# Kernel tuning notes

Hardware: AMD Instinct MI355X
Metric: run time of the kernel (lower is better)

The kernel has to match this reference:

```python
import jax, jax.numpy as jnp
import numpy as np

TAU = 2.0        # spikingjelly LIFNode default tau
VTH = 1.0        # v_threshold
ALPHA = 2.0      # ATan surrogate alpha
NUM_HEADS = 8
N_WIN = 8
TOPK = 4


@jax.custom_vjp
def atan_heaviside(x):
    # spike = H(v - v_th), with ATan surrogate gradient
    return (x >= 0.0).astype(x.dtype)

def _ah_fwd(x):
    return atan_heaviside(x), x

def _ah_bwd(x, g):
    half_pi_alpha = np.float32(np.pi / 2.0 * ALPHA)
    return (g * (ALPHA / 2.0) / (1.0 + (half_pi_alpha * x) ** 2),)

atan_heaviside.defvjp(_ah_fwd, _ah_bwd)


def lif(x):
    """Multi-step LIF over leading time dim. decay_input=True, v_reset=0, detach_reset."""
    def step(v, xt):
        v = v + (xt - v) / TAU                      # charge
        s = atan_heaviside(v - VTH)                 # fire
        v = v * (1.0 - jax.lax.stop_gradient(s))    # hard reset (detached)
        return v, s
    _, spikes = jax.lax.scan(step, jnp.zeros_like(x[0]), x)
    return spikes


def setup_inputs() -> dict:
    key = jax.random.key(0)
    k1, k2, k3, k4, k5 = jax.random.split(key, 5)
    T, B, L, C = 4, 4, 1024, 256
    x = jax.random.normal(k1, (T, B, L, C), dtype=jnp.float32)
    w_qkv = jax.random.normal(k2, (C, 3 * C), dtype=jnp.float32) * (C ** -0.5)
    b_qkv = jax.random.normal(k3, (3 * C,), dtype=jnp.float32) * 0.02
    w_proj = jax.random.normal(k4, (C, C), dtype=jnp.float32) * (C ** -0.5)
    b_proj = jax.random.normal(k5, (C,), dtype=jnp.float32) * 0.02
    return {"x": x, "w_qkv": w_qkv, "b_qkv": b_qkv, "w_proj": w_proj, "b_proj": b_proj}


def reference(x, w_qkv, b_qkv, w_proj, b_proj):
    T, B, L, C = x.shape
    hd = C // NUM_HEADS
    win = L // N_WIN
    scale = hd ** -0.5

    # --- region-level routing (on raw input summed over time) ---
    xs = x.sum(axis=0).reshape(B, N_WIN, win, C)
    region = xs.sum(axis=2)                                  # [B, n_win, C]
    attn_r = jnp.einsum('bnc,bmc->bnm', region, region) * (C ** -0.5)
    _, idx = jax.lax.top_k(attn_r, TOPK)                     # [B, n_win, topk] int32

    # --- qkv + LIF spiking ---
    qkv = x @ w_qkv + b_qkv                                  # [T,B,L,3C]
    q, k, v = jnp.split(qkv, 3, axis=-1)
    q, k, v = lif(q), lif(k), lif(v)
    q = q.reshape(T, B, N_WIN, win, NUM_HEADS, hd)
    k = k.reshape(T, B, N_WIN, win, NUM_HEADS, hd)
    v = v.reshape(T, B, N_WIN, win, NUM_HEADS, hd)

    # --- gather routed KV windows (vectorized; topk-major concat like torch.cat) ---
    b_idx = jnp.arange(B)[:, None, None]                     # [B,1,1]
    k_g = k[:, b_idx, idx].reshape(T, B, N_WIN, TOPK * win, NUM_HEADS, hd)
    v_g = v[:, b_idx, idx].reshape(T, B, N_WIN, TOPK * win, NUM_HEADS, hd)

    # --- windowed attention over gathered keys ---
    attn = jnp.einsum('tbnqhd,tbnkhd->tbnhqk', q, k_g) * scale
    attn = jax.nn.softmax(attn, axis=-1)
    out = jnp.einsum('tbnhqk,tbnkhd->tbnqhd', attn, v_g).reshape(T, B, L, C)

    out = lif(out @ w_proj + b_proj)
    return out
```

## Files before the change

### kernel.cpp

```cpp
#include <hip/hip_runtime.h>
#include <cstdint>
#include <cstddef>

#define TT 4
#define BB 4
#define LL 1024
#define CC 256
#define HH 8
#define HD 32
#define NWIN 8
#define WIN 128
#define TOPKN 4
#define C3 768
#define PKW 24

__global__ __launch_bounds__(64) void region_kernel(const float* __restrict__ x,
                                                    float* __restrict__ region) {
    int bn = blockIdx.x;
    int b = bn >> 3, n = bn & 7;
    int c = blockIdx.y * 64 + threadIdx.x;
    float tot = 0.0f;
    for (int r = 0; r < WIN; ++r) {
        int l = n * WIN + r;
        float s = 0.0f;
        for (int t = 0; t < TT; ++t) {
            s += x[(((size_t)t * BB + b) * LL + l) * CC + c];
        }
        tot += s;
    }
    region[(size_t)bn * CC + c] = tot;
}

__global__ __launch_bounds__(64) void route_kernel(const float* __restrict__ region,
                                                   int* __restrict__ idx) {
    int b = blockIdx.x;
    __shared__ float reg[NWIN][CC];
    __shared__ float attn_r[NWIN][NWIN];
    int tid = threadIdx.x;
    for (int e = tid; e < NWIN * CC; e += 64)
        reg[e >> 8][e & 255] = region[(size_t)b * NWIN * CC + e];
    __syncthreads();
    int n = tid >> 3, m = tid & 7;
    float s = 0.0f;
    for (int c = 0; c < CC; ++c) s += reg[n][c] * reg[m][c];
    attn_r[n][m] = s * 0.0625f;
    __syncthreads();
    if (tid < NWIN) {
        float vals[NWIN];
        for (int m2 = 0; m2 < NWIN; ++m2) vals[m2] = attn_r[tid][m2];
        for (int kk = 0; kk < TOPKN; ++kk) {
            int bi = 0; float bv = vals[0];
            for (int m2 = 1; m2 < NWIN; ++m2) {
                if (vals[m2] > bv) { bv = vals[m2]; bi = m2; }
            }
            idx[(b * NWIN + tid) * TOPKN + kk] = bi;
            vals[bi] = -INFINITY;
        }
    }
}

__global__ __launch_bounds__(256, 3) void gemm_bias128(const float* __restrict__ A,
                                                       const float* __restrict__ W,
                                                       const float* __restrict__ bias,
                                                       float* __restrict__ C,
                                                       int M, int N, int K) {
    const int BM = 128, BN = 128, BK = 16, TM = 8;
    __shared__ float As[BK][BM + 4];
    __shared__ float Bs[BK][136];
    int tid = threadIdx.x;
    int tx = tid & 15, ty = tid >> 4;
    int bm = blockIdx.x * BM, bn = blockIdx.y * BN;
    float acc[TM][8] = {};
    for (int k0 = 0; k0 < K; k0 += BK) {
#pragma unroll
        for (int it = 0; it < 2; ++it) {
            int i = it * 256 + tid;
            int row = i >> 2, kc = (i & 3) * 4;
            float4 v = *(const float4*)(A + (size_t)(bm + row) * K + k0 + kc);
            As[kc + 0][row] = v.x; As[kc + 1][row] = v.y;
            As[kc + 2][row] = v.z; As[kc + 3][row] = v.w;
        }
#pragma unroll
        for (int it = 0; it < 2; ++it) {
            int i = it * 256 + tid;
            int kr = i >> 5, nc = (i & 31) * 4;
            float4 v = *(const float4*)(W + (size_t)(k0 + kr) * N + bn + nc);
            *(float4*)&Bs[kr][nc] = v;
        }
        __syncthreads();
#pragma unroll
        for (int kk = 0; kk < BK; ++kk) {
            float a[TM], bb[8];
            const float4* ap = (const float4*)&As[kk][ty * TM];
            float4 a0 = ap[0], a1 = ap[1];
            a[0]=a0.x; a[1]=a0.y; a[2]=a0.z; a[3]=a0.w;
            a[4]=a1.x; a[5]=a1.y; a[6]=a1.z; a[7]=a1.w;
            float4 b0 = *(const float4*)&Bs[kk][tx * 4];
            float4 b1 = *(const float4*)&Bs[kk][64 + tx * 4];
            bb[0]=b0.x; bb[1]=b0.y; bb[2]=b0.z; bb[3]=b0.w;
            bb[4]=b1.x; bb[5]=b1.y; bb[6]=b1.z; bb[7]=b1.w;
#pragma unroll
            for (int i = 0; i < TM; ++i)
#pragma unroll
                for (int j = 0; j < 8; ++j)
                    acc[i][j] = fmaf(a[i], bb[j], acc[i][j]);
        }
        __syncthreads();
    }
#pragma unroll
    for (int i = 0; i < TM; ++i) {
        int row = bm + ty * TM + i;
        int col0 = bn + tx * 4;
        int col1 = bn + 64 + tx * 4;
        float4 o0 = make_float4(acc[i][0] + bias[col0 + 0], acc[i][1] + bias[col0 + 1],
                                acc[i][2] + bias[col0 + 2], acc[i][3] + bias[col0 + 3]);
        float4 o1 = make_float4(acc[i][4] + bias[col1 + 0], acc[i][5] + bias[col1 + 1],
                                acc[i][6] + bias[col1 + 2], acc[i][7] + bias[col1 + 3]);
        *(float4*)&C[(size_t)row * N + col0] = o0;
        *(float4*)&C[(size_t)row * N + col1] = o1;
    }
}

__global__ __launch_bounds__(256, 4) void gemm_bias64(const float* __restrict__ A,
                                                      const float* __restrict__ W,
                                                      const float* __restrict__ bias,
                                                      float* __restrict__ C,
                                                      int M, int N, int K) {
    const int BM = 64, BN = 64, BK = 16;
    __shared__ float As[BK][BM + 4];
    __shared__ float Bs[BK][72];
    int tid = threadIdx.x;
    int tx = tid & 15, ty = tid >> 4;
    int bm = blockIdx.x * BM, bn = blockIdx.y * BN;
    float acc[4][4] = {};
    for (int k0 = 0; k0 < K; k0 += BK) {
        {
            int row = tid >> 2, kc = (tid & 3) * 4;
            float4 v = *(const float4*)(A + (size_t)(bm + row) * K + k0 + kc);
            As[kc + 0][row] = v.x; As[kc + 1][row] = v.y;
            As[kc + 2][row] = v.z; As[kc + 3][row] = v.w;
        }
        {
            int kr = tid >> 4, nc = (tid & 15) * 4;
            float4 v = *(const float4*)(W + (size_t)(k0 + kr) * N + bn + nc);
            *(float4*)&Bs[kr][nc] = v;
        }
        __syncthreads();
#pragma unroll
        for (int kk = 0; kk < BK; ++kk) {
            float4 av = *(const float4*)&As[kk][ty * 4];
            float4 bv = *(const float4*)&Bs[kk][tx * 4];
            float a[4] = {av.x, av.y, av.z, av.w};
            float bb[4] = {bv.x, bv.y, bv.z, bv.w};
#pragma unroll
            for (int i = 0; i < 4; ++i)
#pragma unroll
                for (int j = 0; j < 4; ++j)
                    acc[i][j] = fmaf(a[i], bb[j], acc[i][j]);
        }
        __syncthreads();
    }
#pragma unroll
    for (int i = 0; i < 4; ++i) {
        int row = bm + ty * 4 + i;
        int col = bn + tx * 4;
        float4 o = make_float4(acc[i][0] + bias[col + 0], acc[i][1] + bias[col + 1],
                               acc[i][2] + bias[col + 2], acc[i][3] + bias[col + 3]);
        *(float4*)&C[(size_t)row * N + col] = o;
    }
}

__global__ __launch_bounds__(256) void lif_kernel(const float* src, float* dst, size_t stride) {
    size_t i = ((size_t)blockIdx.x * blockDim.x + threadIdx.x) * 4;
    float v[4] = {0.f, 0.f, 0.f, 0.f};
    for (int t = 0; t < TT; ++t) {
        float4 xv4 = *(const float4*)(src + (size_t)t * stride + i);
        float xv[4] = {xv4.x, xv4.y, xv4.z, xv4.w};
        float sp[4];
#pragma unroll
        for (int j = 0; j < 4; ++j) {
            v[j] = v[j] + (xv[j] - v[j]) * 0.5f;
            bool fire = (v[j] >= 1.0f);
            sp[j] = fire ? 1.0f : 0.0f;
            v[j] = fire ? 0.0f : v[j];
        }
        *(float4*)(dst + (size_t)t * stride + i) = make_float4(sp[0], sp[1], sp[2], sp[3]);
    }
}

__global__ __launch_bounds__(192) void lif_pack_kernel(const float* __restrict__ qkv,
                                                       uint32_t* __restrict__ pk) {
    int row = blockIdx.x;
    int tid = threadIdx.x;
    int c = tid * 4;
    int wid = tid >> 6;
    int lane = tid & 63;
    const size_t stride = (size_t)BB * LL * C3;
    const float* base = qkv + (size_t)row * C3 + c;

    float v[4] = {0.f, 0.f, 0.f, 0.f};
    for (int t = 0; t < TT; ++t) {
        float4 xv4 = *(const float4*)(base + (size_t)t * stride);
        float xv[4] = {xv4.x, xv4.y, xv4.z, xv4.w};
        bool fire[4];
#pragma unroll
        for (int j = 0; j < 4; ++j) {
            v[j] = v[j] + (xv[j] - v[j]) * 0.5f;
            fire[j] = (v[j] >= 1.0f);
            v[j] = fire[j] ? 0.0f : v[j];
        }
        unsigned long long B0 = __ballot(fire[0]);
        unsigned long long B1 = __ballot(fire[1]);
        unsigned long long B2 = __ballot(fire[2]);
        unsigned long long B3 = __ballot(fire[3]);
        if (lane < 8) {
            uint32_t word = ((uint32_t)(B0 >> (8 * lane)) & 0xFFu)
                          | (((uint32_t)(B1 >> (8 * lane)) & 0xFFu) << 8)
                          | (((uint32_t)(B2 >> (8 * lane)) & 0xFFu) << 16)
                          | (((uint32_t)(B3 >> (8 * lane)) & 0xFFu) << 24);
            pk[((size_t)t * BB * LL + row) * PKW + wid * 8 + lane] = word;
        }
    }
}

__global__ __launch_bounds__(256, 2) void attn_pv(const uint32_t* __restrict__ pk,
                                                  const int* __restrict__ idxws,
                                                  float* __restrict__ out) {
    int bid = blockIdx.x;
    int hp = bid & 3, n = (bid >> 2) & 7, b = (bid >> 5) & 3, t = bid >> 7;
    __shared__ float ptab[33][256];
    __shared__ uint32_t kbs[2][512];
    __shared__ uint32_t vbs[2][512];
    int tid = threadIdx.x;
    int qg = tid & 31, dh = (tid >> 5) & 3, h = tid >> 7;
    int lbase = (t * BB + b) * LL;

    const int* ip = idxws + (b * NWIN + n) * TOPKN;
    int s0r = ip[0], s1r = ip[1], s2r = ip[2], s3r = ip[3];

#pragma unroll 4
    for (int e = tid; e < 1024; e += 256) {
        int hh = e >> 9, kk = e & 511;
        int w = kk >> 7;
        int sw = (w == 0) ? s0r : (w == 1) ? s1r : (w == 2) ? s2r : s3r;
        size_t rowb = (size_t)(lbase + sw * WIN + (kk & 127)) * PKW + hp * 2 + hh;
        kbs[hh][kk] = pk[rowb + 8];
        vbs[hh][kk] = pk[rowb + 16];
    }
    uint32_t qw[4];
#pragma unroll
    for (int j = 0; j < 4; ++j)
        qw[j] = pk[(size_t)(lbase + n * WIN + qg + 32 * j) * PKW + hp * 2 + h];
    __syncthreads();

    const float ALPHA_SC = 0.17677669529663687f;
    {
        int qq = tid & 127, hu = tid >> 7;
        uint32_t qwt = pk[(size_t)(lbase + n * WIN + qq) * PKW + hp * 2 + hu];
        const uint4* kb4u = (const uint4*)kbs[hu];
        int smax = 0;
#pragma unroll 8
        for (int k4 = 0; k4 < 128; ++k4) {
            uint4 w4 = kb4u[k4];
            smax = max(smax, __popc(qwt & w4.x));
            smax = max(smax, __popc(qwt & w4.y));
            smax = max(smax, __popc(qwt & w4.z));
            smax = max(smax, __popc(qwt & w4.w));
        }
        float am = __fmul_rn((float)smax, ALPHA_SC);
        for (int s = 0; s <= 32; ++s)
            ptab[s][tid] = expf(__fsub_rn(__fmul_rn((float)s, ALPHA_SC), am));
        float Z = 0.0f;
#pragma unroll 4
        for (int k4 = 0; k4 < 128; ++k4) {
            uint4 w4 = kb4u[k4];
            Z += ptab[__popc(qwt & w4.x)][tid];
            Z += ptab[__popc(qwt & w4.y)][tid];
            Z += ptab[__popc(qwt & w4.z)][tid];
            Z += ptab[__popc(qwt & w4.w)][tid];
        }
        for (int s = 0; s <= 32; ++s)
            ptab[s][tid] = ptab[s][tid] / Z;
    }
    __syncthreads();

    const uint4* kb4 = (const uint4*)kbs[h];
    const uint32_t* vbh = vbs[h];
    int c0 = h * 128 + qg;
    int po = 2 * dh;
    float acc[4][8];
#pragma unroll
    for (int j = 0; j < 4; ++j)
#pragma unroll
        for (int e = 0; e < 8; ++e) acc[j][e] = 0.0f;

#pragma unroll 1
    for (int g = 0; g < 128; ++g) {
        uint4 kw = kb4[g];
#pragma unroll
        for (int r = 0; r < 4; ++r) {
            uint32_t krow = (r == 0) ? kw.x : (r == 1) ? kw.y : (r == 2) ? kw.z : kw.w;
            uint32_t sh = vbh[g * 4 + r] >> po;
            float P0 = ptab[__popc(qw[0] & krow)][c0];
            float P1 = ptab[__popc(qw[1] & krow)][c0 + 32];
            float P2 = ptab[__popc(qw[2] & krow)][c0 + 64];
            float P3 = ptab[__popc(qw[3] & krow)][c0 + 96];
#pragma unroll
            for (int e = 0; e < 8; ++e) {
                const int offs = (e & 3) * 8 + (e >> 2);
                float vf = (float)((sh >> offs) & 1u);
                acc[0][e] = fmaf(P0, vf, acc[0][e]);
                acc[1][e] = fmaf(P1, vf, acc[1][e]);
                acc[2][e] = fmaf(P2, vf, acc[2][e]);
                acc[3][e] = fmaf(P3, vf, acc[3][e]);
            }
        }
    }

#pragma unroll
    for (int j = 0; j < 4; ++j) {
        size_t ob = (size_t)(lbase + n * WIN + qg + 32 * j) * CC
                    + (hp * 2 + h) * 32 + dh * 8;
        *(float4*)&out[ob]     = make_float4(acc[j][0], acc[j][1], acc[j][2], acc[j][3]);
        *(float4*)&out[ob + 4] = make_float4(acc[j][4], acc[j][5], acc[j][6], acc[j][7]);
    }
}

extern "C" void kernel_launch(void* const* d_in, const int* in_sizes, int n_in,
                              void* d_out, int out_size, void* d_ws, size_t ws_size,
                              hipStream_t stream) {
    const float* x      = (const float*)d_in[0];
    const float* w_qkv  = (const float*)d_in[1];
    const float* b_qkv  = (const float*)d_in[2];
    const float* w_proj = (const float*)d_in[3];
    const float* b_proj = (const float*)d_in[4];
    float* ws = (float*)d_ws;

    float* qkv      = ws;
    float* attn_out = ws + 12582912;
    float* proj     = ws + 16777216;
    uint32_t* pkb   = (uint32_t*)proj;
    float* region   = ws + 20971520;
    int*   idxp     = (int*)(ws + 20979712);
    float* outp     = (float*)d_out;

    region_kernel<<<dim3(BB * NWIN, 4), dim3(64), 0, stream>>>(x, region);
    route_kernel<<<dim3(BB), dim3(64), 0, stream>>>(region, idxp);
    gemm_bias128<<<dim3(128, 6), dim3(256), 0, stream>>>(x, w_qkv, b_qkv, qkv,
                                                         TT * BB * LL, C3, CC);
    lif_pack_kernel<<<dim3(BB * LL), dim3(192), 0, stream>>>(qkv, pkb);
    attn_pv<<<dim3(TT * BB * NWIN * 4), dim3(256), 0, stream>>>(pkb, idxp, attn_out);
    gemm_bias64<<<dim3(256, 4), dim3(256), 0, stream>>>(attn_out, w_proj, b_proj, proj,
                                                        TT * BB * LL, CC, CC);
    lif_kernel<<<dim3(1024), dim3(256), 0, stream>>>(proj, outp, (size_t)BB * LL * CC);
}
```

Measured before the change: 268.6 us.

## Split attention blocks per head to double grid and halve per-thread work

The attention kernel now assigns one head per block instead of two, doubling the grid to 1024 blocks. Each thread handles 64-query groups with 2 query rows instead of 4, and only half the threads build the softmax table. Shared memory shrinks and launch bounds rise to 4 blocks per CU for higher occupancy. V bits are now loaded as uint4 alongside K. The cost is redundant per-block setup, and half the threads sit idle during softmax-table construction.

```diff
diff --git a/kernel.cpp b/kernel.cpp
--- a/kernel.cpp
+++ b/kernel.cpp
@@ -223,45 +223,41 @@
     }
 }
 
-__global__ __launch_bounds__(256, 2) void attn_pv(const uint32_t* __restrict__ pk,
+__global__ __launch_bounds__(256, 4) void attn_pv(const uint32_t* __restrict__ pk,
                                                   const int* __restrict__ idxws,
                                                   float* __restrict__ out) {
     int bid = blockIdx.x;
-    int hp = bid & 3, n = (bid >> 2) & 7, b = (bid >> 5) & 3, t = bid >> 7;
-    __shared__ float ptab[33][256];
-    __shared__ uint32_t kbs[2][512];
-    __shared__ uint32_t vbs[2][512];
-    int tid = threadIdx.x;
-    int qg = tid & 31, dh = (tid >> 5) & 3, h = tid >> 7;
+    int h = bid & 1, hp = (bid >> 1) & 3, n = (bid >> 3) & 7, b = (bid >> 6) & 3, t = bid >> 8;
+    __shared__ float ptab[33][WIN];
+    __shared__ __align__(16) uint32_t kbs[512];
+    __shared__ __align__(16) uint32_t vbs[512];
+    int tid = threadIdx.x;
+    int qg = tid & 63, dh = tid >> 6;
     int lbase = (t * BB + b) * LL;
 
     const int* ip = idxws + (b * NWIN + n) * TOPKN;
     int s0r = ip[0], s1r = ip[1], s2r = ip[2], s3r = ip[3];
 
-#pragma unroll 4
-    for (int e = tid; e < 1024; e += 256) {
-        int hh = e >> 9, kk = e & 511;
-        int w = kk >> 7;
+#pragma unroll 2
+    for (int e = tid; e < 512; e += 256) {
+        int w = e >> 7;
         int sw = (w == 0) ? s0r : (w == 1) ? s1r : (w == 2) ? s2r : s3r;
-        size_t rowb = (size_t)(lbase + sw * WIN + (kk & 127)) * PKW + hp * 2 + hh;
-        kbs[hh][kk] = pk[rowb + 8];
-        vbs[hh][kk] = pk[rowb + 16];
-    }
-    uint32_t qw[4];
-#pragma unroll
-    for (int j = 0; j < 4; ++j)
-        qw[j] = pk[(size_t)(lbase + n * WIN + qg + 32 * j) * PKW + hp * 2 + h];
+        size_t rowb = (size_t)(lbase + sw * WIN + (e & 127)) * PKW + hp * 2 + h;
+        kbs[e] = pk[rowb + 8];
+        vbs[e] = pk[rowb + 16];
+    }
+    uint32_t qw0 = pk[(size_t)(lbase + n * WIN + qg) * PKW + hp * 2 + h];
+    uint32_t qw1 = pk[(size_t)(lbase + n * WIN + qg + 64) * PKW + hp * 2 + h];
     __syncthreads();
 
     const float ALPHA_SC = 0.17677669529663687f;
-    {
-        int qq = tid & 127, hu = tid >> 7;
-        uint32_t qwt = pk[(size_t)(lbase + n * WIN + qq) * PKW + hp * 2 + hu];
-        const uint4* kb4u = (const uint4*)kbs[hu];
+    const uint4* kb4 = (const uint4*)kbs;
+    if (tid < 128) {
+        uint32_t qwt = (tid & 64) ? qw1 : qw0;
         int smax = 0;
 #pragma unroll 8
         for (int k4 = 0; k4 < 128; ++k4) {
-            uint4 w4 = kb4u[k4];
+            uint4 w4 = kb4[k4];
             smax = max(smax, __popc(qwt & w4.x));
             smax = max(smax, __popc(qwt & w4.y));
             smax = max(smax, __popc(qwt & w4.z));
@@ -273,7 +269,7 @@
         float Z = 0.0f;
 #pragma unroll 4
         for (int k4 = 0; k4 < 128; ++k4) {
-            uint4 w4 = kb4u[k4];
+            uint4 w4 = kb4[k4];
             Z += ptab[__popc(qwt & w4.x)][tid];
             Z += ptab[__popc(qwt & w4.y)][tid];
             Z += ptab[__popc(qwt & w4.z)][tid];
@@ -284,46 +280,39 @@
     }
     __syncthreads();
 
-    const uint4* kb4 = (const uint4*)kbs[h];
-    const uint32_t* vbh = vbs[h];
-    int c0 = h * 128 + qg;
+    const uint4* vb4 = (const uint4*)vbs;
     int po = 2 * dh;
-    float acc[4][8];
-#pragma unroll
-    for (int j = 0; j < 4; ++j)
-#pragma unroll
-        for (int e = 0; e < 8; ++e) acc[j][e] = 0.0f;
-
-#pragma unroll 1
+    float acc0[8], acc1[8];
+#pragma unroll
+    for (int e = 0; e < 8; ++e) { acc0[e] = 0.0f; acc1[e] = 0.0f; }
+
+#pragma unroll 2
     for (int g = 0; g < 128; ++g) {
         uint4 kw = kb4[g];
+        uint4 vw = vb4[g];
 #pragma unroll
         for (int r = 0; r < 4; ++r) {
             uint32_t krow = (r == 0) ? kw.x : (r == 1) ? kw.y : (r == 2) ? kw.z : kw.w;
-            uint32_t sh = vbh[g * 4 + r] >> po;
-            float P0 = ptab[__popc(qw[0] & krow)][c0];
-            float P1 = ptab[__popc(qw[1] & krow)][c0 + 32];
-            float P2 = ptab[__popc(qw[2] & krow)][c0 + 64];
-            float P3 = ptab[__popc(qw[3] & krow)][c0 + 96];
+            uint32_t vrow = (r == 0) ? vw.x : (r == 1) ? vw.y : (r == 2) ? vw.z : vw.w;
+            uint32_t sh = vrow >> po;
+            float P0 = ptab[__popc(qw0 & krow)][qg];
+            float P1 = ptab[__popc(qw1 & krow)][qg + 64];
 #pragma unroll
             for (int e = 0; e < 8; ++e) {
                 const int offs = (e & 3) * 8 + (e >> 2);
                 float vf = (float)((sh >> offs) & 1u);
-                acc[0][e] = fmaf(P0, vf, acc[0][e]);
-                acc[1][e] = fmaf(P1, vf, acc[1][e]);
-                acc[2][e] = fmaf(P2, vf, acc[2][e]);
-                acc[3][e] = fmaf(P3, vf, acc[3][e]);
+                acc0[e] = fmaf(P0, vf, acc0[e]);
+                acc1[e] = fmaf(P1, vf, acc1[e]);
             }
         }
     }
 
-#pragma unroll
-    for (int j = 0; j < 4; ++j) {
-        size_t ob = (size_t)(lbase + n * WIN + qg + 32 * j) * CC
-                    + (hp * 2 + h) * 32 + dh * 8;
-        *(float4*)&out[ob]     = make_float4(acc[j][0], acc[j][1], acc[j][2], acc[j][3]);
-        *(float4*)&out[ob + 4] = make_float4(acc[j][4], acc[j][5], acc[j][6], acc[j][7]);
-    }
+    size_t ob0 = (size_t)(lbase + n * WIN + qg) * CC + (hp * 2 + h) * 32 + dh * 8;
+    size_t ob1 = ob0 + (size_t)64 * CC;
+    *(float4*)&out[ob0]     = make_float4(acc0[0], acc0[1], acc0[2], acc0[3]);
+    *(float4*)&out[ob0 + 4] = make_float4(acc0[4], acc0[5], acc0[6], acc0[7]);
+    *(float4*)&out[ob1]     = make_float4(acc1[0], acc1[1], acc1[2], acc1[3]);
+    *(float4*)&out[ob1 + 4] = make_float4(acc1[4], acc1[5], acc1[6], acc1[7]);
 }
 
 extern "C" void kernel_launch(void* const* d_in, const int* in_sizes, int n_in,
@@ -349,7 +338,7 @@
     gemm_bias128<<<dim3(128, 6), dim3(256), 0, stream>>>(x, w_qkv, b_qkv, qkv,
                                                          TT * BB * LL, C3, CC);
     lif_pack_kernel<<<dim3(BB * LL), dim3(192), 0, stream>>>(qkv, pkb);
-    attn_pv<<<dim3(TT * BB * NWIN * 4), dim3(256), 0, stream>>>(pkb, idxp, attn_out);
+    attn_pv<<<dim3(TT * BB * NWIN * 4 * 2), dim3(256), 0, stream>>>(pkb, idxp, attn_out);
     gemm_bias64<<<dim3(256, 4), dim3(256), 0, stream>>>(attn_out, w_proj, b_proj, proj,
                                                         TT * BB * LL, CC, CC);
     lif_kernel<<<dim3(1024), dim3(256), 0, stream>>>(proj, outp, (size_t)BB * LL * CC);
```

Result: slower. 303.1 us (+12.9%).
